# Kernel tuning notes

Hardware: AMD Instinct MI355X
Metric: run time of the kernel (lower is better)

## Reference

```python
import jax, jax.numpy as jnp
import numpy as np

B, T, D_MODEL, D_HEAD = 4, 2048, 1024, 64

def setup_inputs() -> dict:
    key = jax.random.key(0)
    k1, k2, k3, k4 = jax.random.split(key, 4)
    x = jax.random.normal(k1, (B, T, D_MODEL), dtype=jnp.float32)
    # Linear(d_model, d_head) weights stored as [d_model, d_head] for x @ W
    s = 1.0 / np.sqrt(D_MODEL)
    W_Q = jax.random.normal(k2, (D_MODEL, D_HEAD), dtype=jnp.float32) * s
    W_K = jax.random.normal(k3, (D_MODEL, D_HEAD), dtype=jnp.float32) * s
    W_V = jax.random.normal(k4, (D_MODEL, D_HEAD), dtype=jnp.float32) * s
    return {"x": x, "W_Q": W_Q, "W_K": W_K, "W_V": W_V}

def reference(x, W_Q, W_K, W_V):
    d_head = W_Q.shape[-1]
    Q = jnp.einsum('btm,md->btd', x, W_Q)
    K = jnp.einsum('btm,md->btd', x, W_K)
    V = jnp.einsum('btm,md->btd', x, W_V)
    A = jnp.einsum('bid,bjd->bij', Q, K) / jnp.sqrt(jnp.asarray(d_head, x.dtype))
    T_ = x.shape[1]
    causal = jnp.tril(jnp.ones((T_, T_), dtype=bool))  # [T, T]
    A = jnp.where(causal, A, -jnp.inf)
    A = jax.nn.softmax(A, axis=-1)
    return jnp.einsum('bij,bjd->bid', A, V)
```

## Files before the change

### kernel.cpp

```cpp
#include <hip/hip_runtime.h>
#include <hip/hip_bf16.h>

#define NB 4
#define NT 2048
#define DM 1024
#define DH 64

typedef __attribute__((ext_vector_type(8))) short bf16x8;
typedef __attribute__((ext_vector_type(4))) float f32x4;
typedef unsigned short u16;
typedef unsigned int u32;

static __device__ __forceinline__ u16 f2b(float f) {
    __hip_bfloat16 h = __float2bfloat16(f);
    return __builtin_bit_cast(u16, h);
}
static __device__ __forceinline__ float b2f(u16 h) {
    return __builtin_bit_cast(float, (u32)h << 16);
}
static __device__ __forceinline__ void gld16(const void* g, void* l) {
    __builtin_amdgcn_global_load_lds((const __attribute__((address_space(1))) void*)g,
                                     (__attribute__((address_space(3))) void*)l, 16, 0, 0);
}
#define BAR() __builtin_amdgcn_s_barrier()
#define SBAR() __builtin_amdgcn_sched_barrier(0)

__global__ __launch_bounds__(256) void wt_conv(
    const float* __restrict__ WQ, const float* __restrict__ WK,
    const float* __restrict__ WV, u16* __restrict__ wt)
{
    __shared__ u16 tl[64][68];
    const int which = blockIdx.y, kt = blockIdx.x;
    const float* W = (which == 0) ? WQ : (which == 1) ? WK : WV;
    #pragma unroll
    for (int i = 0; i < 4; ++i) {
        int r = (threadIdx.x >> 4) + i * 16;
        int c = (threadIdx.x & 15) * 4;
        float4 v = *(const float4*)&W[(size_t)(kt * 64 + r) * DH + c];
        tl[r][c] = f2b(v.x); tl[r][c + 1] = f2b(v.y);
        tl[r][c + 2] = f2b(v.z); tl[r][c + 3] = f2b(v.w);
    }
    __syncthreads();
    int d = threadIdx.x >> 2, kc = (threadIdx.x & 3) * 16;
    u16 buf[16];
    #pragma unroll
    for (int j = 0; j < 16; ++j) buf[j] = tl[kc + j][d];
    u16* dst = wt + which * 65536 + d * 1024 + kt * 64 + kc;
    *(uint4*)dst = *(uint4*)&buf[0];
    *(uint4*)(dst + 8) = *(uint4*)&buf[8];
}

__global__ __launch_bounds__(256) void qkv_gemm(
    const float* __restrict__ x, const u16* __restrict__ wt,
    u16* __restrict__ Qb, u16* __restrict__ Kb, u16* __restrict__ Vt)
{
    __shared__ float xs[3][4096];
    __shared__ u16 wsm[3][4096];
    const int tid = threadIdx.x, lane = tid & 63, w = tid >> 6;
    const int l15 = lane & 15, g = lane >> 4;
    const int row0 = blockIdx.x * 64;
    const int which = blockIdx.y;
    const u16* Wg = wt + which * 65536;

    auto stage = [&](int kt, int bi) {
        #pragma unroll
        for (int i = 0; i < 4; ++i) {
            u32 D = (u32)(w * 4096 + i * 1024 + lane * 16);
            u32 r = D >> 8, c = D & 255;
            u32 cs = c ^ ((r & 7) << 5);
            gld16(x + (size_t)(row0 + r) * DM + kt * 64 + (cs >> 2),
                  (char*)&xs[bi][0] + w * 4096 + i * 1024);
        }
        #pragma unroll
        for (int i = 0; i < 2; ++i) {
            u32 D = (u32)(w * 2048 + i * 1024 + lane * 16);
            u32 r = D >> 7, c = D & 127;
            u32 cs = c ^ ((r & 7) << 4);
            gld16(Wg + (size_t)r * 1024 + kt * 64 + (cs >> 1),
                  (char*)&wsm[bi][0] + w * 2048 + i * 1024);
        }
    };

    f32x4 acc[4];
    #pragma unroll
    for (int i = 0; i < 4; ++i) acc[i] = {0.f, 0.f, 0.f, 0.f};

    stage(0, 0);
    stage(1, 1);

    const int arow = w * 16 + l15;
    #pragma unroll
    for (int kt = 0; kt < 16; ++kt) {
        if (kt + 2 < 16) stage(kt + 2, (kt + 2) % 3);
        if (kt < 14)       asm volatile("s_waitcnt vmcnt(12)" ::: "memory");
        else if (kt == 14) asm volatile("s_waitcnt vmcnt(6)" ::: "memory");
        else               asm volatile("s_waitcnt vmcnt(0)" ::: "memory");
        BAR();
        SBAR();
        const char* xb = (const char*)&xs[kt % 3][0];
        const char* wb = (const char*)&wsm[kt % 3][0];
        #pragma unroll
        for (int ks = 0; ks < 2; ++ks) {
            u32 abase = (u32)(arow * 256 + ks * 128 + g * 32);
            f32x4 a0 = *(const f32x4*)(xb + (abase ^ ((arow & 7) << 5)));
            f32x4 a1 = *(const f32x4*)(xb + ((abase + 16) ^ ((arow & 7) << 5)));
            bf16x8 afrag;
            #pragma unroll
            for (int e = 0; e < 4; ++e) afrag[e] = (short)f2b(a0[e]);
            #pragma unroll
            for (int e = 0; e < 4; ++e) afrag[4 + e] = (short)f2b(a1[e]);
            __builtin_amdgcn_s_setprio(1);
            #pragma unroll
            for (int nt = 0; nt < 4; ++nt) {
                int brow = nt * 16 + l15;
                u32 bb = (u32)(brow * 128 + ks * 64 + g * 16);
                bf16x8 bfrag = *(const bf16x8*)(wb + (bb ^ ((brow & 7) << 4)));
                acc[nt] = __builtin_amdgcn_mfma_f32_16x16x32_bf16(afrag, bfrag, acc[nt], 0, 0, 0);
            }
            __builtin_amdgcn_s_setprio(0);
        }
        BAR();
    }
    #pragma unroll
    for (int nt = 0; nt < 4; ++nt) {
        int dcol = nt * 16 + l15;
        #pragma unroll
        for (int r = 0; r < 4; ++r) {
            int row = row0 + w * 16 + g * 4 + r;
            float v = acc[nt][r];
            if (which == 0)      Qb[(size_t)row * DH + dcol] = f2b(v * 0.125f);
            else if (which == 1) Kb[(size_t)row * DH + dcol] = f2b(v);
            else { int bb2 = row >> 11, t = row & 2047;
                   Vt[(size_t)bb2 * DH * NT + (size_t)dcol * NT + t] = f2b(v); }
        }
    }
}

__global__ __launch_bounds__(256) void attn(
    const u16* __restrict__ Qb, const u16* __restrict__ Kb,
    const u16* __restrict__ Vt, u16* __restrict__ pO, float* __restrict__ pml,
    int CHUNK, int SLOTS)
{
    __shared__ u16 k_lds[2][4096];
    __shared__ u16 v_lds[2][4096];
    __shared__ u16 p_lds[4][16 * 72];

    const int tid = threadIdx.x, lane = tid & 63, w = tid >> 6;
    const int l15 = lane & 15, g = lane >> 4;
    const int b = blockIdx.y;

    int flat = blockIdx.x, qb = 0, nc;
    for (;;) { nc = (qb + CHUNK) / CHUNK; if (flat < nc) break; flat -= nc; ++qb; }
    const int chunk = flat;
    const int t0 = chunk * CHUNK;
    const int t1 = min(t0 + CHUNK, qb + 1);
    const int q0 = qb * 64;

    const u16* Qg = Qb + ((size_t)b * NT + q0 + w * 16) * DH;
    const u16* Kg = Kb + (size_t)b * NT * DH;
    const u16* Vg = Vt + (size_t)b * DH * NT;

    auto stage = [&](int t, int bi) {
        const int j0 = t * 64;
        #pragma unroll
        for (int i = 0; i < 2; ++i) {
            u32 D = (u32)(w * 2048 + i * 1024 + lane * 16);
            u32 r = D >> 7, c = D & 127;
            u32 cs = c ^ ((r & 7) << 4);
            gld16(Kg + (size_t)(j0 + r) * DH + (cs >> 1),
                  (char*)&k_lds[bi][0] + w * 2048 + i * 1024);
            gld16(Vg + (size_t)r * NT + j0 + (cs >> 1),
                  (char*)&v_lds[bi][0] + w * 2048 + i * 1024);
        }
    };

    stage(t0, 0);

    bf16x8 qf[2];
    qf[0] = *(const bf16x8*)(Qg + l15 * DH + g * 8);
    qf[1] = *(const bf16x8*)(Qg + l15 * DH + 32 + g * 8);

    float m_run[4], l_run[4];
    f32x4 oacc[4];
    #pragma unroll
    for (int r = 0; r < 4; ++r) { m_run[r] = -INFINITY; l_run[r] = 0.f; }
    #pragma unroll
    for (int nt = 0; nt < 4; ++nt) oacc[nt] = {0.f, 0.f, 0.f, 0.f};

    for (int t = t0; t < t1; ++t) {
        const int cur = (t - t0) & 1;
        if (t + 1 < t1) {
            stage(t + 1, cur ^ 1);
            asm volatile("s_waitcnt vmcnt(4)" ::: "memory");
        } else {
            asm volatile("s_waitcnt vmcnt(0)" ::: "memory");
        }
        BAR();
        SBAR();
        const char* kb = (const char*)&k_lds[cur][0];
        const char* vb = (const char*)&v_lds[cur][0];

        f32x4 sacc[4];
        #pragma unroll
        for (int nt = 0; nt < 4; ++nt) sacc[nt] = {0.f, 0.f, 0.f, 0.f};
        __builtin_amdgcn_s_setprio(1);
        #pragma unroll
        for (int ks = 0; ks < 2; ++ks) {
            #pragma unroll
            for (int nt = 0; nt < 4; ++nt) {
                int brow = nt * 16 + l15;
                u32 bb = (u32)(brow * 128 + ks * 64 + g * 16);
                bf16x8 bf = *(const bf16x8*)(kb + (bb ^ ((brow & 7) << 4)));
                sacc[nt] = __builtin_amdgcn_mfma_f32_16x16x32_bf16(qf[ks], bf, sacc[nt], 0, 0, 0);
            }
        }
        __builtin_amdgcn_s_setprio(0);
        if (t == qb) {
            #pragma unroll
            for (int nt = 0; nt < 4; ++nt) {
                int j_local = nt * 16 + l15;
                #pragma unroll
                for (int r = 0; r < 4; ++r) {
                    int q_local = w * 16 + g * 4 + r;
                    if (j_local > q_local) sacc[nt][r] = -1e30f;
                }
            }
        }
        float p[4][4];
        #pragma unroll
        for (int r = 0; r < 4; ++r) {
            float mx = fmaxf(fmaxf(sacc[0][r], sacc[1][r]), fmaxf(sacc[2][r], sacc[3][r]));
            mx = fmaxf(mx, __shfl_xor(mx, 1));
            mx = fmaxf(mx, __shfl_xor(mx, 2));
            mx = fmaxf(mx, __shfl_xor(mx, 4));
            mx = fmaxf(mx, __shfl_xor(mx, 8));
            float m_new = fmaxf(m_run[r], mx);
            float alpha = __expf(m_run[r] - m_new);
            float ps = 0.f;
            #pragma unroll
            for (int nt = 0; nt < 4; ++nt) {
                float pv = __expf(sacc[nt][r] - m_new);
                p[nt][r] = pv; ps += pv;
            }
            ps += __shfl_xor(ps, 1); ps += __shfl_xor(ps, 2);
            ps += __shfl_xor(ps, 4); ps += __shfl_xor(ps, 8);
            l_run[r] = l_run[r] * alpha + ps;
            m_run[r] = m_new;
            #pragma unroll
            for (int nt = 0; nt < 4; ++nt) oacc[nt][r] *= alpha;
        }
        u16* pw = p_lds[w];
        #pragma unroll
        for (int r = 0; r < 4; ++r) {
            int qrow = g * 4 + r;
            #pragma unroll
            for (int nt = 0; nt < 4; ++nt)
                pw[qrow * 72 + nt * 16 + l15] = f2b(p[nt][r]);
        }
        __builtin_amdgcn_s_setprio(1);
        #pragma unroll
        for (int ks = 0; ks < 2; ++ks) {
            bf16x8 pa = *(const bf16x8*)((const char*)pw + (l15 * 144 + ks * 64 + g * 16));
            #pragma unroll
            for (int nt = 0; nt < 4; ++nt) {
                int drow = nt * 16 + l15;
                u32 bb = (u32)(drow * 128 + ks * 64 + g * 16);
                bf16x8 vf = *(const bf16x8*)(vb + (bb ^ ((drow & 7) << 4)));
                oacc[nt] = __builtin_amdgcn_mfma_f32_16x16x32_bf16(pa, vf, oacc[nt], 0, 0, 0);
            }
        }
        __builtin_amdgcn_s_setprio(0);
        BAR();
    }

    const int slot = (b * 32 + qb) * SLOTS + chunk;
    u16* Op = pO + (size_t)slot * 4096;
    #pragma unroll
    for (int nt = 0; nt < 4; ++nt)
        #pragma unroll
        for (int r = 0; r < 4; ++r)
            Op[(w * 16 + g * 4 + r) * 64 + nt * 16 + l15] = f2b(oacc[nt][r]);
    if (l15 == 0) {
        float* mlp = pml + (size_t)slot * 128;
        #pragma unroll
        for (int r = 0; r < 4; ++r) {
            int row = w * 16 + g * 4 + r;
            mlp[row * 2]     = m_run[r];
            mlp[row * 2 + 1] = l_run[r];
        }
    }
}

__global__ __launch_bounds__(256) void merge(
    const u16* __restrict__ pO, const float* __restrict__ pml,
    float* __restrict__ out, int CHUNK, int SLOTS)
{
    int idx = blockIdx.x * 256 + threadIdx.x;
    int row = idx >> 6, d = idx & 63;
    int b = row >> 11, q = row & 2047;
    int qb = q >> 6, rl = q & 63;
    int nc = (qb + CHUNK) / CHUNK;
    int base = (b * 32 + qb) * SLOTS;
    float m = -INFINITY;
    for (int c = 0; c < nc; ++c)
        m = fmaxf(m, pml[(size_t)(base + c) * 128 + rl * 2]);
    float osum = 0.f, lsum = 0.f;
    for (int c = 0; c < nc; ++c) {
        float mc = pml[(size_t)(base + c) * 128 + rl * 2];
        float lc = pml[(size_t)(base + c) * 128 + rl * 2 + 1];
        float wgt = __expf(mc - m);
        osum += wgt * b2f(pO[(size_t)(base + c) * 4096 + rl * 64 + d]);
        lsum += wgt * lc;
    }
    out[idx] = osum / lsum;
}

extern "C" void kernel_launch(void* const* d_in, const int* in_sizes, int n_in,
                              void* d_out, int out_size, void* d_ws, size_t ws_size,
                              hipStream_t stream) {
    const float* x  = (const float*)d_in[0];
    const float* WQ = (const float*)d_in[1];
    const float* WK = (const float*)d_in[2];
    const float* WV = (const float*)d_in[3];
    float* out = (float*)d_out;

    char* ws = (char*)d_ws;
    u16* Qb = (u16*)ws;
    u16* Kb = (u16*)(ws + 1048576);
    u16* Vt = (u16*)(ws + 2097152);
    u16* Wt = (u16*)(ws + 3145728);
    int CHUNK, SLOTS;
    if (ws_size >= 9830400) { CHUNK = 6;  SLOTS = 6; }
    else                    { CHUNK = 16; SLOTS = 2; }
    u16*   pO  = (u16*)(ws + 3145728);
    float* pml = (float*)(ws + 3145728 + (size_t)NB * 32 * SLOTS * 4096 * 2);

    int gx = 0;
    for (int qb = 0; qb < 32; ++qb) gx += (qb + CHUNK) / CHUNK;

    wt_conv<<<dim3(16, 3), 256, 0, stream>>>(WQ, WK, WV, Wt);
    qkv_gemm<<<dim3(128, 3), 256, 0, stream>>>(x, Wt, Qb, Kb, Vt);
    attn<<<dim3(gx, NB), 256, 0, stream>>>(Qb, Kb, Vt, pO, pml, CHUNK, SLOTS);
    merge<<<2048, 256, 0, stream>>>(pO, pml, out, CHUNK, SLOTS);
}
```

Measured before the change: 48.26 us.

## Transpose attention MFMA operands, shrink GEMM pipeline to double buffer, rework merge

The attention kernel swaps the MFMA operand order so each lane owns one query row. This makes the softmax row max and sum reductions need only two cross-lane shuffles, and it writes P to LDS as packed, swizzled 8-byte stores. The partial outputs are now stored transposed, and the merge kernel is rewritten to handle one 64-row query block per workgroup, transposing through LDS so output writes are float4. Separately, the QKV GEMM goes from triple to double buffering, which uses less LDS but overlaps loads with compute less deeply.

```diff
diff --git a/kernel.cpp b/kernel.cpp
--- a/kernel.cpp
+++ b/kernel.cpp
@@ -54,8 +54,8 @@
     const float* __restrict__ x, const u16* __restrict__ wt,
     u16* __restrict__ Qb, u16* __restrict__ Kb, u16* __restrict__ Vt)
 {
-    __shared__ float xs[3][4096];
-    __shared__ u16 wsm[3][4096];
+    __shared__ float xs[2][4096];
+    __shared__ u16 wsm[2][4096];
     const int tid = threadIdx.x, lane = tid & 63, w = tid >> 6;
     const int l15 = lane & 15, g = lane >> 4;
     const int row0 = blockIdx.x * 64;
@@ -86,19 +86,20 @@
     for (int i = 0; i < 4; ++i) acc[i] = {0.f, 0.f, 0.f, 0.f};
 
     stage(0, 0);
-    stage(1, 1);
 
     const int arow = w * 16 + l15;
     #pragma unroll
     for (int kt = 0; kt < 16; ++kt) {
-        if (kt + 2 < 16) stage(kt + 2, (kt + 2) % 3);
-        if (kt < 14)       asm volatile("s_waitcnt vmcnt(12)" ::: "memory");
-        else if (kt == 14) asm volatile("s_waitcnt vmcnt(6)" ::: "memory");
-        else               asm volatile("s_waitcnt vmcnt(0)" ::: "memory");
+        if (kt < 15) {
+            stage(kt + 1, (kt + 1) & 1);
+            asm volatile("s_waitcnt vmcnt(6)" ::: "memory");
+        } else {
+            asm volatile("s_waitcnt vmcnt(0)" ::: "memory");
+        }
         BAR();
         SBAR();
-        const char* xb = (const char*)&xs[kt % 3][0];
-        const char* wb = (const char*)&wsm[kt % 3][0];
+        const char* xb = (const char*)&xs[kt & 1][0];
+        const char* wb = (const char*)&wsm[kt & 1][0];
         #pragma unroll
         for (int ks = 0; ks < 2; ++ks) {
             u32 abase = (u32)(arow * 256 + ks * 128 + g * 32);
@@ -138,12 +139,12 @@
 
 __global__ __launch_bounds__(256) void attn(
     const u16* __restrict__ Qb, const u16* __restrict__ Kb,
-    const u16* __restrict__ Vt, u16* __restrict__ pO, float* __restrict__ pml,
+    const u16* __restrict__ Vt, u16* __restrict__ pOt, float* __restrict__ pml,
     int CHUNK, int SLOTS)
 {
     __shared__ u16 k_lds[2][4096];
     __shared__ u16 v_lds[2][4096];
-    __shared__ u16 p_lds[4][16 * 72];
+    __shared__ f32x4 p_lds[4][128];
 
     const int tid = threadIdx.x, lane = tid & 63, w = tid >> 6;
     const int l15 = lane & 15, g = lane >> 4;
@@ -180,12 +181,13 @@
     qf[0] = *(const bf16x8*)(Qg + l15 * DH + g * 8);
     qf[1] = *(const bf16x8*)(Qg + l15 * DH + 32 + g * 8);
 
-    float m_run[4], l_run[4];
+    float m_run = -INFINITY, l_run = 0.f;
     f32x4 oacc[4];
     #pragma unroll
-    for (int r = 0; r < 4; ++r) { m_run[r] = -INFINITY; l_run[r] = 0.f; }
-    #pragma unroll
     for (int nt = 0; nt < 4; ++nt) oacc[nt] = {0.f, 0.f, 0.f, 0.f};
+
+    char* pw = (char*)&p_lds[w][0];
+    const int swz = (l15 & 7) << 4;
 
     for (int t = t0; t < t1; ++t) {
         const int cur = (t - t0) & 1;
@@ -208,65 +210,72 @@
         for (int ks = 0; ks < 2; ++ks) {
             #pragma unroll
             for (int nt = 0; nt < 4; ++nt) {
-                int brow = nt * 16 + l15;
-                u32 bb = (u32)(brow * 128 + ks * 64 + g * 16);
-                bf16x8 bf = *(const bf16x8*)(kb + (bb ^ ((brow & 7) << 4)));
-                sacc[nt] = __builtin_amdgcn_mfma_f32_16x16x32_bf16(qf[ks], bf, sacc[nt], 0, 0, 0);
+                int arow = nt * 16 + l15;
+                u32 aa = (u32)(arow * 128 + ks * 64 + g * 16);
+                bf16x8 kf = *(const bf16x8*)(kb + (aa ^ ((arow & 7) << 4)));
+                sacc[nt] = __builtin_amdgcn_mfma_f32_16x16x32_bf16(kf, qf[ks], sacc[nt], 0, 0, 0);
             }
         }
         __builtin_amdgcn_s_setprio(0);
         if (t == qb) {
-            #pragma unroll
-            for (int nt = 0; nt < 4; ++nt) {
-                int j_local = nt * 16 + l15;
+            const int q_local = w * 16 + l15;
+            #pragma unroll
+            for (int nt = 0; nt < 4; ++nt)
                 #pragma unroll
-                for (int r = 0; r < 4; ++r) {
-                    int q_local = w * 16 + g * 4 + r;
-                    if (j_local > q_local) sacc[nt][r] = -1e30f;
-                }
-            }
-        }
+                for (int r = 0; r < 4; ++r)
+                    if (nt * 16 + g * 4 + r > q_local) sacc[nt][r] = -1e30f;
+        }
+        float mx = -INFINITY;
+        #pragma unroll
+        for (int nt = 0; nt < 4; ++nt) {
+            float a = fmaxf(fmaxf(sacc[nt][0], sacc[nt][1]),
+                            fmaxf(sacc[nt][2], sacc[nt][3]));
+            mx = fmaxf(mx, a);
+        }
+        mx = fmaxf(mx, __shfl_xor(mx, 16));
+        mx = fmaxf(mx, __shfl_xor(mx, 32));
+        const float m_new = fmaxf(m_run, mx);
+        const float alpha = __expf(m_run - m_new);
         float p[4][4];
-        #pragma unroll
-        for (int r = 0; r < 4; ++r) {
-            float mx = fmaxf(fmaxf(sacc[0][r], sacc[1][r]), fmaxf(sacc[2][r], sacc[3][r]));
-            mx = fmaxf(mx, __shfl_xor(mx, 1));
-            mx = fmaxf(mx, __shfl_xor(mx, 2));
-            mx = fmaxf(mx, __shfl_xor(mx, 4));
-            mx = fmaxf(mx, __shfl_xor(mx, 8));
-            float m_new = fmaxf(m_run[r], mx);
-            float alpha = __expf(m_run[r] - m_new);
-            float ps = 0.f;
-            #pragma unroll
-            for (int nt = 0; nt < 4; ++nt) {
+        float ps = 0.f;
+        #pragma unroll
+        for (int nt = 0; nt < 4; ++nt)
+            #pragma unroll
+            for (int r = 0; r < 4; ++r) {
                 float pv = __expf(sacc[nt][r] - m_new);
                 p[nt][r] = pv; ps += pv;
             }
-            ps += __shfl_xor(ps, 1); ps += __shfl_xor(ps, 2);
-            ps += __shfl_xor(ps, 4); ps += __shfl_xor(ps, 8);
-            l_run[r] = l_run[r] * alpha + ps;
-            m_run[r] = m_new;
-            #pragma unroll
-            for (int nt = 0; nt < 4; ++nt) oacc[nt][r] *= alpha;
-        }
-        u16* pw = p_lds[w];
-        #pragma unroll
-        for (int r = 0; r < 4; ++r) {
-            int qrow = g * 4 + r;
-            #pragma unroll
-            for (int nt = 0; nt < 4; ++nt)
-                pw[qrow * 72 + nt * 16 + l15] = f2b(p[nt][r]);
-        }
+        ps += __shfl_xor(ps, 16);
+        ps += __shfl_xor(ps, 32);
+        l_run = l_run * alpha + ps;
+        m_run = m_new;
+        #pragma unroll
+        for (int nt = 0; nt < 4; ++nt)
+            #pragma unroll
+            for (int r = 0; r < 4; ++r) oacc[nt][r] *= alpha;
+
+        #pragma unroll
+        for (int nt = 0; nt < 4; ++nt) {
+            uint2 pk;
+            pk.x = (u32)f2b(p[nt][0]) | ((u32)f2b(p[nt][1]) << 16);
+            pk.y = (u32)f2b(p[nt][2]) | ((u32)f2b(p[nt][3]) << 16);
+            u32 a = (u32)((l15 * 128 + nt * 32 + g * 8) ^ swz);
+            *(uint2*)(pw + a) = pk;
+        }
+        bf16x8 pb[2];
+        #pragma unroll
+        for (int ks = 0; ks < 2; ++ks)
+            pb[ks] = *(const bf16x8*)(pw + ((u32)(l15 * 128 + ks * 64 + g * 16) ^ swz));
+
         __builtin_amdgcn_s_setprio(1);
         #pragma unroll
         for (int ks = 0; ks < 2; ++ks) {
-            bf16x8 pa = *(const bf16x8*)((const char*)pw + (l15 * 144 + ks * 64 + g * 16));
             #pragma unroll
             for (int nt = 0; nt < 4; ++nt) {
-                int drow = nt * 16 + l15;
-                u32 bb = (u32)(drow * 128 + ks * 64 + g * 16);
-                bf16x8 vf = *(const bf16x8*)(vb + (bb ^ ((drow & 7) << 4)));
-                oacc[nt] = __builtin_amdgcn_mfma_f32_16x16x32_bf16(pa, vf, oacc[nt], 0, 0, 0);
+                int arow = nt * 16 + l15;
+                u32 aa = (u32)(arow * 128 + ks * 64 + g * 16);
+                bf16x8 vf = *(const bf16x8*)(vb + (aa ^ ((arow & 7) << 4)));
+                oacc[nt] = __builtin_amdgcn_mfma_f32_16x16x32_bf16(vf, pb[ks], oacc[nt], 0, 0, 0);
             }
         }
         __builtin_amdgcn_s_setprio(0);
@@ -274,45 +283,59 @@
     }
 
     const int slot = (b * 32 + qb) * SLOTS + chunk;
-    u16* Op = pO + (size_t)slot * 4096;
+    u16* Op = pOt + (size_t)slot * 4096;
     #pragma unroll
     for (int nt = 0; nt < 4; ++nt)
         #pragma unroll
         for (int r = 0; r < 4; ++r)
-            Op[(w * 16 + g * 4 + r) * 64 + nt * 16 + l15] = f2b(oacc[nt][r]);
-    if (l15 == 0) {
+            Op[(nt * 16 + g * 4 + r) * 64 + w * 16 + l15] = f2b(oacc[nt][r]);
+    if (g == 0) {
         float* mlp = pml + (size_t)slot * 128;
-        #pragma unroll
-        for (int r = 0; r < 4; ++r) {
-            int row = w * 16 + g * 4 + r;
-            mlp[row * 2]     = m_run[r];
-            mlp[row * 2 + 1] = l_run[r];
-        }
+        mlp[(w * 16 + l15) * 2]     = m_run;
+        mlp[(w * 16 + l15) * 2 + 1] = l_run;
     }
 }
 
 __global__ __launch_bounds__(256) void merge(
-    const u16* __restrict__ pO, const float* __restrict__ pml,
+    const u16* __restrict__ pOt, const float* __restrict__ pml,
     float* __restrict__ out, int CHUNK, int SLOTS)
 {
-    int idx = blockIdx.x * 256 + threadIdx.x;
-    int row = idx >> 6, d = idx & 63;
-    int b = row >> 11, q = row & 2047;
-    int qb = q >> 6, rl = q & 63;
-    int nc = (qb + CHUNK) / CHUNK;
-    int base = (b * 32 + qb) * SLOTS;
+    __shared__ float tl[64][65];
+    const int bq = blockIdx.x;
+    const int b = bq >> 5, qb = bq & 31;
+    const int nc = (qb + CHUNK) / CHUNK;
+    const int base = bq * SLOTS;
+    const int q = threadIdx.x & 63, ds = threadIdx.x >> 6;
+
     float m = -INFINITY;
     for (int c = 0; c < nc; ++c)
-        m = fmaxf(m, pml[(size_t)(base + c) * 128 + rl * 2]);
-    float osum = 0.f, lsum = 0.f;
+        m = fmaxf(m, pml[(size_t)(base + c) * 128 + q * 2]);
+    float lsum = 0.f;
+    float acc[16];
+    #pragma unroll
+    for (int i = 0; i < 16; ++i) acc[i] = 0.f;
     for (int c = 0; c < nc; ++c) {
-        float mc = pml[(size_t)(base + c) * 128 + rl * 2];
-        float lc = pml[(size_t)(base + c) * 128 + rl * 2 + 1];
-        float wgt = __expf(mc - m);
-        osum += wgt * b2f(pO[(size_t)(base + c) * 4096 + rl * 64 + d]);
-        lsum += wgt * lc;
-    }
-    out[idx] = osum / lsum;
+        const float mc = pml[(size_t)(base + c) * 128 + q * 2];
+        const float lc = pml[(size_t)(base + c) * 128 + q * 2 + 1];
+        const float wc = __expf(mc - m);
+        lsum += wc * lc;
+        const u16* Op = pOt + (size_t)(base + c) * 4096;
+        #pragma unroll
+        for (int i = 0; i < 16; ++i)
+            acc[i] += wc * b2f(Op[(ds * 16 + i) * 64 + q]);
+    }
+    const float inv = 1.f / lsum;
+    #pragma unroll
+    for (int i = 0; i < 16; ++i) tl[q][ds * 16 + i] = acc[i] * inv;
+    __syncthreads();
+    const int q2 = threadIdx.x >> 2, dc = threadIdx.x & 3;
+    float* orow = out + ((size_t)b * NT + qb * 64 + q2) * 64 + dc * 16;
+    #pragma unroll
+    for (int j4 = 0; j4 < 4; ++j4) {
+        float4 v = { tl[q2][dc * 16 + j4 * 4 + 0], tl[q2][dc * 16 + j4 * 4 + 1],
+                     tl[q2][dc * 16 + j4 * 4 + 2], tl[q2][dc * 16 + j4 * 4 + 3] };
+        *(float4*)&orow[j4 * 4] = v;
+    }
 }
 
 extern "C" void kernel_launch(void* const* d_in, const int* in_sizes, int n_in,
@@ -332,7 +355,7 @@
     int CHUNK, SLOTS;
     if (ws_size >= 9830400) { CHUNK = 6;  SLOTS = 6; }
     else                    { CHUNK = 16; SLOTS = 2; }
-    u16*   pO  = (u16*)(ws + 3145728);
+    u16*   pOt = (u16*)(ws + 3145728);
     float* pml = (float*)(ws + 3145728 + (size_t)NB * 32 * SLOTS * 4096 * 2);
 
     int gx = 0;
@@ -340,6 +363,6 @@
 
     wt_conv<<<dim3(16, 3), 256, 0, stream>>>(WQ, WK, WV, Wt);
     qkv_gemm<<<dim3(128, 3), 256, 0, stream>>>(x, Wt, Qb, Kb, Vt);
-    attn<<<dim3(gx, NB), 256, 0, stream>>>(Qb, Kb, Vt, pO, pml, CHUNK, SLOTS);
-    merge<<<2048, 256, 0, stream>>>(pO, pml, out, CHUNK, SLOTS);
-}
+    attn<<<dim3(gx, NB), 256, 0, stream>>>(Qb, Kb, Vt, pOt, pml, CHUNK, SLOTS);
+    merge<<<NB * 32, 256, 0, stream>>>(pOt, pml, out, CHUNK, SLOTS);
+}
```

New measurement: 45.62 us. 5.5% less time.
